# Performance work log

Hardware: AMD Instinct MI355X
Metric: run time of the kernel (lower is better)

Reference implementation:

```python
import jax, jax.numpy as jnp
import numpy as np


def cv_sigmoid(z):
    # split sigmoid: sigmoid(Re) + i*sigmoid(Im)
    return jax.nn.sigmoid(z.real) + 1j * jax.nn.sigmoid(z.imag)


def cv_polar_tanh(z):
    # tanh on magnitude, phase preserved: tanh(|z|) * z / |z|
    mag = jnp.abs(z)
    safe = jnp.where(mag == 0, 1.0, mag)
    return (jnp.tanh(mag) / safe).astype(z.dtype) * z


def setup_inputs() -> dict:
    key = jax.random.key(0)
    B, D, H = 16384, 512, 512
    ks = jax.random.split(key, 12)
    names = ['x_re', 'x_im', 'h_re', 'h_im', 'Wx_re', 'Wx_im', 'Wh_re', 'Wh_im', 'bx_re', 'bx_im', 'bh_re', 'bh_im']
    shapes = [(B, D), (B, D), (B, H), (B, H), (3, H, D), (3, H, D), (3, H, H), (3, H, H), (3, H), (3, H), (3, H), (3, H)]
    out = {}
    for n, s, k in zip(names, shapes, ks):
        scale = 1.0 if n[0] in ('x', 'h') else (1.0 / np.sqrt(s[-1]))
        out[n] = jax.random.normal(k, s, dtype=jnp.float32) * scale
    return out


def reference(x_re, x_im, h_re, h_im, Wx_re, Wx_im, Wh_re, Wh_im, bx_re, bx_im, bh_re, bh_im):
    x = (x_re + 1j * x_im).astype(jnp.complex64)   # [B, D]
    h = (h_re + 1j * h_im).astype(jnp.complex64)   # [B, H]
    Wx = (Wx_re + 1j * Wx_im).astype(jnp.complex64)  # [3, H, D] (z, r, h)
    Wh = (Wh_re + 1j * Wh_im).astype(jnp.complex64)  # [3, H, H]
    bx = (bx_re + 1j * bx_im).astype(jnp.complex64)  # [3, H]
    bh = (bh_re + 1j * bh_im).astype(jnp.complex64)  # [3, H]

    # input projections for all three gates at once: [3, B, H]
    px = jnp.einsum('bd,khd->kbh', x, Wx) + bx[:, None, :]
    # hidden projections for z and r gates
    pz = jnp.einsum('bh,gh->bg', h, Wh[0]) + bh[0]
    pr = jnp.einsum('bh,gh->bg', h, Wh[1]) + bh[1]

    z = cv_sigmoid(px[0] + pz)
    r = cv_sigmoid(px[1] + pr)

    ph = jnp.einsum('bh,gh->bg', r * h, Wh[2]) + bh[2]
    h_tilde = cv_polar_tanh(px[2] + ph)

    h_new = (1.0 - z) * h + z * h_tilde  # [B, H] complex
    # return as stacked real/imag float tensor [B, H, 2]
    return jnp.stack([h_new.real, h_new.imag], axis=-1)
```

## Files before the change

### kernel.cpp

```cpp
#include <hip/hip_runtime.h>
#include <hip/hip_bf16.h>

typedef __bf16 bf16_t;
typedef __bf16 bf16x8 __attribute__((ext_vector_type(8)));
typedef __bf16 bf16x4 __attribute__((ext_vector_type(4)));
typedef float f32x4 __attribute__((ext_vector_type(4)));


__device__ __forceinline__ void gl_lds16(const bf16_t* g, bf16_t* l) {
  __builtin_amdgcn_global_load_lds(
      (const __attribute__((address_space(1))) void*)g,
      (__attribute__((address_space(3))) void*)l, 16, 0, 0);
}

__device__ __forceinline__ float fast_sigmoid(float x) {
  return 1.0f / (1.0f + __expf(-x));
}

__global__ void pack_A(const float* __restrict__ x_re, const float* __restrict__ x_im,
                       const float* __restrict__ h_re, const float* __restrict__ h_im,
                       bf16_t* __restrict__ A) {
  int q = blockIdx.x * blockDim.x + threadIdx.x;
  int i4 = q << 2;
  int b = i4 >> 11;
  int k = i4 & 2047;
  int seg = k >> 9;
  int off = k & 511;
  const float* s = (seg == 0) ? x_re : (seg == 1) ? x_im : (seg == 2) ? h_re : h_im;
  const float4 v = *(const float4*)(s + (size_t)b * 512 + off);
  bf16x4 o = { (bf16_t)v.x, (bf16_t)v.y, (bf16_t)v.z, (bf16_t)v.w };
  *(bf16x4*)(A + (size_t)b * 2048 + k) = o;
}

__global__ void pack_W(const float* __restrict__ Wx_re, const float* __restrict__ Wx_im,
                       const float* __restrict__ Wh_re, const float* __restrict__ Wh_im,
                       bf16_t* __restrict__ W1t) {
  int q = blockIdx.x * blockDim.x + threadIdx.x;
  int n = q >> 9;
  int k2 = (q & 511) << 2;
  int g = n >> 10;
  int j = (n & 1023) >> 1;
  int p = n & 1;
  int pair = k2 >> 10;
  const float* Wre = pair ? Wh_re : Wx_re;
  const float* Wim = pair ? Wh_im : Wx_im;
  int klocal = k2 & 1023;
  int half = klocal >> 9;
  int off = klocal & 511;
  size_t sidx = ((size_t)g * 512 + j) * 512 + off;
  const float* s = (half == 0) ? (p ? Wim : Wre) : (p ? Wre : Wim);
  float sgn = (half == 1 && p == 0) ? -1.0f : 1.0f;
  float4 v = *(const float4*)(s + sidx);
  bf16x4 o = { (bf16_t)(sgn * v.x), (bf16_t)(sgn * v.y),
               (bf16_t)(sgn * v.z), (bf16_t)(sgn * v.w) };
  *(bf16x4*)(W1t + (size_t)n * 2048 + k2) = o;
}

template <int MODE>
__launch_bounds__(512, 2)
__global__ void gemm_fused(const bf16_t* __restrict__ A, const bf16_t* __restrict__ W,
                           int LDA, int LDW,
                           bf16_t* __restrict__ zbuf, bf16_t* __restrict__ A2,
                           float* __restrict__ outbuf,
                           const float* __restrict__ h_re, const float* __restrict__ h_im,
                           const float* __restrict__ bx_re, const float* __restrict__ bx_im,
                           const float* __restrict__ bh_re, const float* __restrict__ bh_im) {
  __shared__ __align__(16) bf16_t As[2][256 * 64];
  __shared__ __align__(16) bf16_t Bs[2][256 * 64];

  const int bid = blockIdx.x;
  const int xcd = bid & 7;
  const int idx = bid >> 3;
  const int ntile = idx >> 3;
  const int mtile = (xcd << 3) + (idx & 7);
  const int m0 = mtile * 256;
  const int n0 = ntile * 256;
  const int region = (MODE == 1) ? (ntile >> 2) : 2;
  const int nKT = 32;

  const int tid = threadIdx.x;
  const int lane = tid & 63;
  const int w = tid >> 6;
  const int wr = w >> 2;
  const int wc = w & 3;

  const int rb = tid >> 3;
  const int cc = tid & 7;
  const int cs = cc ^ (rb & 7);
  const bf16_t* Ag = A + (size_t)(m0 + rb) * LDA + cs * 8;
  const bf16_t* Rg = A2 + (size_t)(m0 + rb) * 1024 + cs * 8;
  const bf16_t* Wg = W + (size_t)(n0 + rb) * LDW + cs * 8;

#define STAGE_A(s, bufi, kt2) do {                                            \
    const bf16_t* _g;                                                         \
    if (MODE == 2 && (kt2) >= 16)                                             \
      _g = Rg + (size_t)(s) * 64 * 1024 + ((kt2) - 16) * 64;                  \
    else                                                                      \
      _g = Ag + (size_t)(s) * 64 * LDA + (kt2) * 64;                          \
    gl_lds16(_g, &As[bufi][tid * 8 + (s) * 4096]);                            \
  } while (0)
#define STAGE_B(s, bufi, kt2) \
  gl_lds16(Wg + (size_t)(s) * 64 * LDW + (kt2) * 64, &Bs[bufi][tid * 8 + (s) * 4096])

  const int quad = lane >> 4, lrow = lane & 15;
  int aOff[8], bOff[4];
#pragma unroll
  for (int mt = 0; mt < 8; ++mt) {
    const int r = wr * 128 + mt * 16 + lrow;
    aOff[mt] = r * 64 + ((quad ^ (r & 7)) << 3);
  }
#pragma unroll
  for (int nt = 0; nt < 4; ++nt) {
    const int r = wc * 64 + nt * 16 + lrow;
    bOff[nt] = r * 64 + ((quad ^ (r & 7)) << 3);
  }

  f32x4 acc[8][4] = {};

  STAGE_B(0, 0, 0); STAGE_B(1, 0, 0); STAGE_B(2, 0, 0); STAGE_B(3, 0, 0);
  STAGE_A(0, 0, 0); STAGE_A(2, 0, 0);
  STAGE_A(1, 0, 0); STAGE_A(3, 0, 0);
  asm volatile("s_waitcnt vmcnt(2)" ::: "memory");
  __builtin_amdgcn_s_barrier();

  for (int kt = 0; kt < nKT; ++kt) {
    const int b = kt & 1;
    const bf16_t* Ab = As[b];
    const bf16_t* Bb = Bs[b];
    const bool s1 = (kt + 1 < nKT);

    bf16x8 bk[4], bk1[4], af[4];

#pragma unroll
    for (int nt = 0; nt < 4; ++nt) bk[nt] = *(const bf16x8*)(Bb + bOff[nt]);
#pragma unroll
    for (int i = 0; i < 4; ++i) af[i] = *(const bf16x8*)(Ab + aOff[i]);
    if (s1) { STAGE_B(0, b ^ 1, kt + 1); STAGE_B(1, b ^ 1, kt + 1); }
    __builtin_amdgcn_s_barrier();
    asm volatile("s_waitcnt lgkmcnt(0)" ::: "memory");
    __builtin_amdgcn_s_setprio(1);
#pragma unroll
    for (int i = 0; i < 4; ++i)
#pragma unroll
      for (int nt = 0; nt < 4; ++nt)
        acc[i][nt] = __builtin_amdgcn_mfma_f32_16x16x32_bf16(af[i], bk[nt], acc[i][nt], 0, 0, 0);
    __builtin_amdgcn_s_setprio(0);
    if (s1) asm volatile("s_waitcnt vmcnt(2)" ::: "memory");
    else    asm volatile("s_waitcnt vmcnt(0)" ::: "memory");
    __builtin_amdgcn_s_barrier();

#pragma unroll
    for (int i = 0; i < 4; ++i) af[i] = *(const bf16x8*)(Ab + aOff[4 + i]);
    if (s1) { STAGE_B(2, b ^ 1, kt + 1); STAGE_B(3, b ^ 1, kt + 1); }
    __builtin_amdgcn_s_barrier();
    asm volatile("s_waitcnt lgkmcnt(0)" ::: "memory");
    __builtin_amdgcn_s_setprio(1);
#pragma unroll
    for (int i = 0; i < 4; ++i)
#pragma unroll
      for (int nt = 0; nt < 4; ++nt)
        acc[4 + i][nt] = __builtin_amdgcn_mfma_f32_16x16x32_bf16(af[i], bk[nt], acc[4 + i][nt], 0, 0, 0);
    __builtin_amdgcn_s_setprio(0);
    __builtin_amdgcn_s_barrier();

#pragma unroll
    for (int nt = 0; nt < 4; ++nt) bk1[nt] = *(const bf16x8*)(Bb + (bOff[nt] ^ 32));
#pragma unroll
    for (int i = 0; i < 4; ++i) af[i] = *(const bf16x8*)(Ab + (aOff[i] ^ 32));
    if (s1) { STAGE_A(0, b ^ 1, kt + 1); STAGE_A(2, b ^ 1, kt + 1); }
    __builtin_amdgcn_s_barrier();
    asm volatile("s_waitcnt lgkmcnt(0)" ::: "memory");
    __builtin_amdgcn_s_setprio(1);
#pragma unroll
    for (int i = 0; i < 4; ++i)
#pragma unroll
      for (int nt = 0; nt < 4; ++nt)
        acc[i][nt] = __builtin_amdgcn_mfma_f32_16x16x32_bf16(af[i], bk1[nt], acc[i][nt], 0, 0, 0);
    __builtin_amdgcn_s_setprio(0);
    __builtin_amdgcn_s_barrier();

#pragma unroll
    for (int i = 0; i < 4; ++i) af[i] = *(const bf16x8*)(Ab + (aOff[4 + i] ^ 32));
    if (s1) { STAGE_A(1, b ^ 1, kt + 1); STAGE_A(3, b ^ 1, kt + 1); }
    __builtin_amdgcn_s_barrier();
    asm volatile("s_waitcnt lgkmcnt(0)" ::: "memory");
    __builtin_amdgcn_s_setprio(1);
#pragma unroll
    for (int i = 0; i < 4; ++i)
#pragma unroll
      for (int nt = 0; nt < 4; ++nt)
        acc[4 + i][nt] = __builtin_amdgcn_mfma_f32_16x16x32_bf16(af[i], bk1[nt], acc[4 + i][nt], 0, 0, 0);
    __builtin_amdgcn_s_setprio(0);
    if (s1) asm volatile("s_waitcnt vmcnt(2)" ::: "memory");
    __builtin_amdgcn_s_barrier();
  }
#undef STAGE_A
#undef STAGE_B

#pragma unroll
  for (int mt = 0; mt < 8; ++mt) {
#pragma unroll
    for (int nt = 0; nt < 4; ++nt) {
#pragma unroll
      for (int rg = 0; rg < 4; ++rg) {
        const int m = m0 + wr * 128 + mt * 16 + quad * 4 + rg;
        const int n = n0 + wc * 64 + nt * 16 + lrow;
        float v = acc[mt][nt][rg];
        const int p = n & 1;
        const int cj = n & 1023;
        const int j = cj >> 1;
        const float bias = p ? (bx_im[region * 512 + j] + bh_im[region * 512 + j])
                             : (bx_re[region * 512 + j] + bh_re[region * 512 + j]);
        const float val = v + bias;

        if (MODE == 1) {
          if (region == 0) {
            zbuf[(size_t)m * 1024 + cj] = (bf16_t)fast_sigmoid(val);
          } else {
            float rv = fast_sigmoid(val);
            float ro = __shfl_xor(rv, 1, 64);
            float hp = p ? h_im[(size_t)m * 512 + j] : h_re[(size_t)m * 512 + j];
            float ho = __shfl_xor(hp, 1, 64);
            float rh = (p == 0) ? (rv * hp - ro * ho) : (ro * hp + rv * ho);
            A2[(size_t)m * 1024 + p * 512 + j] = (bf16_t)rh;
          }
        } else {
          float u = val;
          float uo = __shfl_xor(u, 1, 64);
          float mag = sqrtf(u * u + uo * uo);
          float mm = fminf(mag, 20.0f);
          float e = __expf(2.0f * mm);
          float th = (e - 1.0f) / (e + 1.0f);
          float s = (mag == 0.0f) ? 0.0f : (th / mag);
          float hto = s * u;
          float htd = s * uo;
          float zv = (float)zbuf[(size_t)m * 1024 + cj];
          float zo = __shfl_xor(zv, 1, 64);
          float hp = p ? h_im[(size_t)m * 512 + j] : h_re[(size_t)m * 512 + j];
          float ho = __shfl_xor(hp, 1, 64);
          float res;
          if (p == 0)
            res = (1.0f - zv) * hp + zo * ho + zv * hto - zo * htd;
          else
            res = (1.0f - zo) * hp - zv * ho + zo * hto + zv * htd;
          outbuf[(size_t)m * 1024 + cj] = res;
        }
      }
    }
  }
}

extern "C" void kernel_launch(void* const* d_in, const int* in_sizes, int n_in,
                              void* d_out, int out_size, void* d_ws, size_t ws_size,
                              hipStream_t stream) {
  const float* x_re  = (const float*)d_in[0];
  const float* x_im  = (const float*)d_in[1];
  const float* h_re  = (const float*)d_in[2];
  const float* h_im  = (const float*)d_in[3];
  const float* Wx_re = (const float*)d_in[4];
  const float* Wx_im = (const float*)d_in[5];
  const float* Wh_re = (const float*)d_in[6];
  const float* Wh_im = (const float*)d_in[7];
  const float* bx_re = (const float*)d_in[8];
  const float* bx_im = (const float*)d_in[9];
  const float* bh_re = (const float*)d_in[10];
  const float* bh_im = (const float*)d_in[11];
  float* out = (float*)d_out;

  char* ws = (char*)d_ws;
  bf16_t* A_big = (bf16_t*)(ws);
  bf16_t* W1t   = (bf16_t*)(ws + 67108864);
  bf16_t* A2    = (bf16_t*)(ws + 79691776);
  bf16_t* zbuf  = (bf16_t*)(ws + 113246208);

  pack_A<<<32768, 256, 0, stream>>>(x_re, x_im, h_re, h_im, A_big);
  pack_W<<<6144, 256, 0, stream>>>(Wx_re, Wx_im, Wh_re, Wh_im, W1t);
  gemm_fused<1><<<512, 512, 0, stream>>>(A_big, W1t, 2048, 2048,
      zbuf, A2, out, h_re, h_im, bx_re, bx_im, bh_re, bh_im);
  gemm_fused<2><<<256, 512, 0, stream>>>(A_big, W1t + (size_t)2048 * 2048, 2048, 2048,
      zbuf, A2, out, h_re, h_im, bx_re, bx_im, bh_re, bh_im);
}
```

Before: 606.3 us.

## Merge pack kernels and use 1024-thread GEMM blocks with simpler K loop

```diff
diff --git a/kernel.cpp b/kernel.cpp
--- a/kernel.cpp
+++ b/kernel.cpp
@@ -17,47 +17,48 @@
   return 1.0f / (1.0f + __expf(-x));
 }
 
-__global__ void pack_A(const float* __restrict__ x_re, const float* __restrict__ x_im,
-                       const float* __restrict__ h_re, const float* __restrict__ h_im,
-                       bf16_t* __restrict__ A) {
-  int q = blockIdx.x * blockDim.x + threadIdx.x;
-  int i4 = q << 2;
-  int b = i4 >> 11;
-  int k = i4 & 2047;
-  int seg = k >> 9;
-  int off = k & 511;
-  const float* s = (seg == 0) ? x_re : (seg == 1) ? x_im : (seg == 2) ? h_re : h_im;
-  const float4 v = *(const float4*)(s + (size_t)b * 512 + off);
-  bf16x4 o = { (bf16_t)v.x, (bf16_t)v.y, (bf16_t)v.z, (bf16_t)v.w };
-  *(bf16x4*)(A + (size_t)b * 2048 + k) = o;
-}
-
-__global__ void pack_W(const float* __restrict__ Wx_re, const float* __restrict__ Wx_im,
-                       const float* __restrict__ Wh_re, const float* __restrict__ Wh_im,
-                       bf16_t* __restrict__ W1t) {
-  int q = blockIdx.x * blockDim.x + threadIdx.x;
-  int n = q >> 9;
-  int k2 = (q & 511) << 2;
-  int g = n >> 10;
-  int j = (n & 1023) >> 1;
-  int p = n & 1;
-  int pair = k2 >> 10;
-  const float* Wre = pair ? Wh_re : Wx_re;
-  const float* Wim = pair ? Wh_im : Wx_im;
-  int klocal = k2 & 1023;
-  int half = klocal >> 9;
-  int off = klocal & 511;
-  size_t sidx = ((size_t)g * 512 + j) * 512 + off;
-  const float* s = (half == 0) ? (p ? Wim : Wre) : (p ? Wre : Wim);
-  float sgn = (half == 1 && p == 0) ? -1.0f : 1.0f;
-  float4 v = *(const float4*)(s + sidx);
-  bf16x4 o = { (bf16_t)(sgn * v.x), (bf16_t)(sgn * v.y),
-               (bf16_t)(sgn * v.z), (bf16_t)(sgn * v.w) };
-  *(bf16x4*)(W1t + (size_t)n * 2048 + k2) = o;
+__global__ void pack_AW(const float* __restrict__ x_re, const float* __restrict__ x_im,
+                        const float* __restrict__ h_re, const float* __restrict__ h_im,
+                        const float* __restrict__ Wx_re, const float* __restrict__ Wx_im,
+                        const float* __restrict__ Wh_re, const float* __restrict__ Wh_im,
+                        bf16_t* __restrict__ A, bf16_t* __restrict__ W1t) {
+  const int bid = blockIdx.x;
+  if (bid < 32768) {
+    int q = bid * 256 + threadIdx.x;
+    int i4 = q << 2;
+    int b = i4 >> 11;
+    int k = i4 & 2047;
+    int seg = k >> 9;
+    int off = k & 511;
+    const float* s = (seg == 0) ? x_re : (seg == 1) ? x_im : (seg == 2) ? h_re : h_im;
+    const float4 v = *(const float4*)(s + (size_t)b * 512 + off);
+    bf16x4 o = { (bf16_t)v.x, (bf16_t)v.y, (bf16_t)v.z, (bf16_t)v.w };
+    *(bf16x4*)(A + (size_t)b * 2048 + k) = o;
+  } else {
+    int q = (bid - 32768) * 256 + threadIdx.x;
+    int n = q >> 9;
+    int k2 = (q & 511) << 2;
+    int g = n >> 10;
+    int j = (n & 1023) >> 1;
+    int p = n & 1;
+    int pair = k2 >> 10;
+    const float* Wre = pair ? Wh_re : Wx_re;
+    const float* Wim = pair ? Wh_im : Wx_im;
+    int klocal = k2 & 1023;
+    int half = klocal >> 9;
+    int off = klocal & 511;
+    size_t sidx = ((size_t)g * 512 + j) * 512 + off;
+    const float* s = (half == 0) ? (p ? Wim : Wre) : (p ? Wre : Wim);
+    float sgn = (half == 1 && p == 0) ? -1.0f : 1.0f;
+    float4 v = *(const float4*)(s + sidx);
+    bf16x4 o = { (bf16_t)(sgn * v.x), (bf16_t)(sgn * v.y),
+                 (bf16_t)(sgn * v.z), (bf16_t)(sgn * v.w) };
+    *(bf16x4*)(W1t + (size_t)n * 2048 + k2) = o;
+  }
 }
 
 template <int MODE>
-__launch_bounds__(512, 2)
+__launch_bounds__(1024, 4)
 __global__ void gemm_fused(const bf16_t* __restrict__ A, const bf16_t* __restrict__ W,
                            int LDA, int LDW,
                            bf16_t* __restrict__ zbuf, bf16_t* __restrict__ A2,
@@ -94,19 +95,19 @@
 #define STAGE_A(s, bufi, kt2) do {                                            \
     const bf16_t* _g;                                                         \
     if (MODE == 2 && (kt2) >= 16)                                             \
-      _g = Rg + (size_t)(s) * 64 * 1024 + ((kt2) - 16) * 64;                  \
+      _g = Rg + (size_t)(s) * 128 * 1024 + ((kt2) - 16) * 64;                 \
     else                                                                      \
-      _g = Ag + (size_t)(s) * 64 * LDA + (kt2) * 64;                          \
-    gl_lds16(_g, &As[bufi][tid * 8 + (s) * 4096]);                            \
+      _g = Ag + (size_t)(s) * 128 * LDA + (kt2) * 64;                         \
+    gl_lds16(_g, &As[bufi][tid * 8 + (s) * 8192]);                            \
   } while (0)
 #define STAGE_B(s, bufi, kt2) \
-  gl_lds16(Wg + (size_t)(s) * 64 * LDW + (kt2) * 64, &Bs[bufi][tid * 8 + (s) * 4096])
+  gl_lds16(Wg + (size_t)(s) * 128 * LDW + (kt2) * 64, &Bs[bufi][tid * 8 + (s) * 8192])
 
   const int quad = lane >> 4, lrow = lane & 15;
-  int aOff[8], bOff[4];
-#pragma unroll
-  for (int mt = 0; mt < 8; ++mt) {
-    const int r = wr * 128 + mt * 16 + lrow;
+  int aOff[4], bOff[4];
+#pragma unroll
+  for (int mt = 0; mt < 4; ++mt) {
+    const int r = wr * 64 + mt * 16 + lrow;
     aOff[mt] = r * 64 + ((quad ^ (r & 7)) << 3);
   }
 #pragma unroll
@@ -115,12 +116,11 @@
     bOff[nt] = r * 64 + ((quad ^ (r & 7)) << 3);
   }
 
-  f32x4 acc[8][4] = {};
-
-  STAGE_B(0, 0, 0); STAGE_B(1, 0, 0); STAGE_B(2, 0, 0); STAGE_B(3, 0, 0);
-  STAGE_A(0, 0, 0); STAGE_A(2, 0, 0);
-  STAGE_A(1, 0, 0); STAGE_A(3, 0, 0);
-  asm volatile("s_waitcnt vmcnt(2)" ::: "memory");
+  f32x4 acc[4][4] = {};
+
+  STAGE_B(0, 0, 0); STAGE_B(1, 0, 0);
+  STAGE_A(0, 0, 0); STAGE_A(1, 0, 0);
+  asm volatile("s_waitcnt vmcnt(0)" ::: "memory");
   __builtin_amdgcn_s_barrier();
 
   for (int kt = 0; kt < nKT; ++kt) {
@@ -129,81 +129,50 @@
     const bf16_t* Bb = Bs[b];
     const bool s1 = (kt + 1 < nKT);
 
-    bf16x8 bk[4], bk1[4], af[4];
-
-#pragma unroll
-    for (int nt = 0; nt < 4; ++nt) bk[nt] = *(const bf16x8*)(Bb + bOff[nt]);
-#pragma unroll
-    for (int i = 0; i < 4; ++i) af[i] = *(const bf16x8*)(Ab + aOff[i]);
-    if (s1) { STAGE_B(0, b ^ 1, kt + 1); STAGE_B(1, b ^ 1, kt + 1); }
-    __builtin_amdgcn_s_barrier();
-    asm volatile("s_waitcnt lgkmcnt(0)" ::: "memory");
+    if (s1) {
+      STAGE_B(0, b ^ 1, kt + 1); STAGE_B(1, b ^ 1, kt + 1);
+      STAGE_A(0, b ^ 1, kt + 1); STAGE_A(1, b ^ 1, kt + 1);
+    }
+
+    bf16x8 ak[4], bk[4];
+
+#pragma unroll
+    for (int i = 0; i < 4; ++i) bk[i] = *(const bf16x8*)(Bb + bOff[i]);
+#pragma unroll
+    for (int i = 0; i < 4; ++i) ak[i] = *(const bf16x8*)(Ab + aOff[i]);
     __builtin_amdgcn_s_setprio(1);
 #pragma unroll
     for (int i = 0; i < 4; ++i)
 #pragma unroll
-      for (int nt = 0; nt < 4; ++nt)
-        acc[i][nt] = __builtin_amdgcn_mfma_f32_16x16x32_bf16(af[i], bk[nt], acc[i][nt], 0, 0, 0);
+      for (int j2 = 0; j2 < 4; ++j2)
+        acc[i][j2] = __builtin_amdgcn_mfma_f32_16x16x32_bf16(ak[i], bk[j2], acc[i][j2], 0, 0, 0);
     __builtin_amdgcn_s_setprio(0);
-    if (s1) asm volatile("s_waitcnt vmcnt(2)" ::: "memory");
-    else    asm volatile("s_waitcnt vmcnt(0)" ::: "memory");
-    __builtin_amdgcn_s_barrier();
-
-#pragma unroll
-    for (int i = 0; i < 4; ++i) af[i] = *(const bf16x8*)(Ab + aOff[4 + i]);
-    if (s1) { STAGE_B(2, b ^ 1, kt + 1); STAGE_B(3, b ^ 1, kt + 1); }
-    __builtin_amdgcn_s_barrier();
-    asm volatile("s_waitcnt lgkmcnt(0)" ::: "memory");
+
+#pragma unroll
+    for (int i = 0; i < 4; ++i) bk[i] = *(const bf16x8*)(Bb + (bOff[i] ^ 32));
+#pragma unroll
+    for (int i = 0; i < 4; ++i) ak[i] = *(const bf16x8*)(Ab + (aOff[i] ^ 32));
     __builtin_amdgcn_s_setprio(1);
 #pragma unroll
     for (int i = 0; i < 4; ++i)
 #pragma unroll
-      for (int nt = 0; nt < 4; ++nt)
-        acc[4 + i][nt] = __builtin_amdgcn_mfma_f32_16x16x32_bf16(af[i], bk[nt], acc[4 + i][nt], 0, 0, 0);
+      for (int j2 = 0; j2 < 4; ++j2)
+        acc[i][j2] = __builtin_amdgcn_mfma_f32_16x16x32_bf16(ak[i], bk[j2], acc[i][j2], 0, 0, 0);
     __builtin_amdgcn_s_setprio(0);
-    __builtin_amdgcn_s_barrier();
-
-#pragma unroll
-    for (int nt = 0; nt < 4; ++nt) bk1[nt] = *(const bf16x8*)(Bb + (bOff[nt] ^ 32));
-#pragma unroll
-    for (int i = 0; i < 4; ++i) af[i] = *(const bf16x8*)(Ab + (aOff[i] ^ 32));
-    if (s1) { STAGE_A(0, b ^ 1, kt + 1); STAGE_A(2, b ^ 1, kt + 1); }
-    __builtin_amdgcn_s_barrier();
-    asm volatile("s_waitcnt lgkmcnt(0)" ::: "memory");
-    __builtin_amdgcn_s_setprio(1);
-#pragma unroll
-    for (int i = 0; i < 4; ++i)
-#pragma unroll
-      for (int nt = 0; nt < 4; ++nt)
-        acc[i][nt] = __builtin_amdgcn_mfma_f32_16x16x32_bf16(af[i], bk1[nt], acc[i][nt], 0, 0, 0);
-    __builtin_amdgcn_s_setprio(0);
-    __builtin_amdgcn_s_barrier();
-
-#pragma unroll
-    for (int i = 0; i < 4; ++i) af[i] = *(const bf16x8*)(Ab + (aOff[4 + i] ^ 32));
-    if (s1) { STAGE_A(1, b ^ 1, kt + 1); STAGE_A(3, b ^ 1, kt + 1); }
-    __builtin_amdgcn_s_barrier();
-    asm volatile("s_waitcnt lgkmcnt(0)" ::: "memory");
-    __builtin_amdgcn_s_setprio(1);
-#pragma unroll
-    for (int i = 0; i < 4; ++i)
-#pragma unroll
-      for (int nt = 0; nt < 4; ++nt)
-        acc[4 + i][nt] = __builtin_amdgcn_mfma_f32_16x16x32_bf16(af[i], bk1[nt], acc[4 + i][nt], 0, 0, 0);
-    __builtin_amdgcn_s_setprio(0);
-    if (s1) asm volatile("s_waitcnt vmcnt(2)" ::: "memory");
+
+    if (s1) asm volatile("s_waitcnt vmcnt(0)" ::: "memory");
     __builtin_amdgcn_s_barrier();
   }
 #undef STAGE_A
 #undef STAGE_B
 
 #pragma unroll
-  for (int mt = 0; mt < 8; ++mt) {
+  for (int mt = 0; mt < 4; ++mt) {
 #pragma unroll
     for (int nt = 0; nt < 4; ++nt) {
 #pragma unroll
       for (int rg = 0; rg < 4; ++rg) {
-        const int m = m0 + wr * 128 + mt * 16 + quad * 4 + rg;
+        const int m = m0 + wr * 64 + mt * 16 + quad * 4 + rg;
         const int n = n0 + wc * 64 + nt * 16 + lrow;
         float v = acc[mt][nt][rg];
         const int p = n & 1;
@@ -273,10 +242,10 @@
   bf16_t* A2    = (bf16_t*)(ws + 79691776);
   bf16_t* zbuf  = (bf16_t*)(ws + 113246208);
 
-  pack_A<<<32768, 256, 0, stream>>>(x_re, x_im, h_re, h_im, A_big);
-  pack_W<<<6144, 256, 0, stream>>>(Wx_re, Wx_im, Wh_re, Wh_im, W1t);
-  gemm_fused<1><<<512, 512, 0, stream>>>(A_big, W1t, 2048, 2048,
+  pack_AW<<<38912, 256, 0, stream>>>(x_re, x_im, h_re, h_im,
+      Wx_re, Wx_im, Wh_re, Wh_im, A_big, W1t);
+  gemm_fused<1><<<512, 1024, 0, stream>>>(A_big, W1t, 2048, 2048,
       zbuf, A2, out, h_re, h_im, bx_re, bx_im, bh_re, bh_im);
-  gemm_fused<2><<<256, 512, 0, stream>>>(A_big, W1t + (size_t)2048 * 2048, 2048, 2048,
+  gemm_fused<2><<<256, 1024, 0, stream>>>(A_big, W1t + (size_t)2048 * 2048, 2048, 2048,
       zbuf, A2, out, h_re, h_im, bx_re, bx_im, bh_re, bh_im);
 }
```

Result: faster. 511.8 us (-15.6%).
